# Kernel optimization log

Measured on AMD Instinct MI355X. Metric: run time of the kernel, lower is better.

Reference implementation:

```python
import jax, jax.numpy as jnp
import numpy as np

B, N, D, H = 2, 2048, 128, 16  # batch, seq, per-head dim, heads
ALL = D * H


def setup_inputs() -> dict:
    key = jax.random.key(0)
    ks = jax.random.split(key, 12)
    s = 0.02
    x = jax.random.normal(ks[0], (B, N, D), dtype=jnp.float32)
    mask = jax.random.randint(ks[1], (B, N), 0, 2, dtype=jnp.int32)
    Wq = jax.random.normal(ks[2], (D, ALL), dtype=jnp.float32) * s
    bq = jnp.zeros((ALL,), dtype=jnp.float32)
    Wk = jax.random.normal(ks[3], (D, ALL), dtype=jnp.float32) * s
    bk = jnp.zeros((ALL,), dtype=jnp.float32)
    Wv = jax.random.normal(ks[4], (D, ALL), dtype=jnp.float32) * s
    bv = jnp.zeros((ALL,), dtype=jnp.float32)
    Wo = jax.random.normal(ks[5], (ALL, D), dtype=jnp.float32) * s
    bo = jnp.zeros((D,), dtype=jnp.float32)
    return {"x": x, "mask": mask, "Wq": Wq, "bq": bq, "Wk": Wk, "bk": bk,
            "Wv": Wv, "bv": bv, "Wo": Wo, "bo": bo}


def reference(x, mask, Wq, bq, Wk, bk, Wv, bv, Wo, bo):
    b, n, d = x.shape
    h = ALL // d
    # project and split heads: [b, n, h, d] -> [b, h, n, d]
    q = (x @ Wq + bq).reshape(b, n, h, d).transpose(0, 2, 1, 3)
    k = (x @ Wk + bk).reshape(b, n, h, d).transpose(0, 2, 1, 3)
    v = (x @ Wv + bv).reshape(b, n, h, d).transpose(0, 2, 1, 3)
    scores = jnp.einsum('bhqd,bhkd->bhqk', q, k) / jnp.sqrt(jnp.float32(d))
    # key mask: [b,1,1,n]
    scores = jnp.where(mask[:, None, None, :] == 0, -jnp.inf, scores)
    attn = jax.nn.softmax(scores, axis=-1)  # dropout p=0.0 -> identity
    out = jnp.einsum('bhqk,bhkd->bhqd', attn, v)
    # query mask: [b,1,n,1]
    out = jnp.where(mask[:, None, :, None] == 0, 0.0, out)
    out = out.transpose(0, 2, 1, 3).reshape(b, n, h * d)
    return out @ Wo + bo
```

## Files before the change

### kernel.cpp

```cpp
#include <hip/hip_runtime.h>
#include <hip/hip_bf16.h>

#define B_   2
#define N_   2048
#define D_   128
#define H_   16
#define ALL_ 2048
#define M_   (B_*N_)
#define BH_  (B_*H_)

typedef __bf16 bf16;
typedef __bf16 bf16x8 __attribute__((ext_vector_type(8)));
typedef __bf16 bf16x4 __attribute__((ext_vector_type(4)));
typedef float  floatx4 __attribute__((ext_vector_type(4)));

#define MFMA32K(a,b,c) __builtin_amdgcn_mfma_f32_16x16x32_bf16((a),(b),(c),0,0,0)

__device__ inline void load_lds16(const bf16* g, bf16* l) {
    __builtin_amdgcn_global_load_lds((const __attribute__((address_space(1))) void*)g,
                                     (__attribute__((address_space(3))) void*)l, 16, 0, 0);
}

#define WAITCNT_VM(n) ((0xF << 8) | (0x7 << 4) | (n))


__global__ __launch_bounds__(256) void prep_weights(const float* __restrict__ x,
                                                    const float* __restrict__ Wq,
                                                    const float* __restrict__ Wk,
                                                    const float* __restrict__ Wv,
                                                    const float* __restrict__ Wo,
                                                    const int* __restrict__ mask,
                                                    bf16* __restrict__ Wqf,
                                                    bf16* __restrict__ Wkf,
                                                    bf16* __restrict__ Wvf,
                                                    bf16* __restrict__ Wof,
                                                    bf16* __restrict__ xf,
                                                    float* __restrict__ mbias) {
    __shared__ bf16 pw[16896];
    int bid = blockIdx.x, t = threadIdx.x;
    int lane = t & 63, wave = t >> 6;
    int lrow = lane & 15, quad = lane >> 4;

    if (bid < 192) {
        int m = bid / 64, rest = bid % 64;
        int cg = rest >> 1, kh = rest & 1;
        const float* W = (m == 0) ? Wq : (m == 1) ? Wk : Wv;
        bf16* Wf       = (m == 0) ? Wqf : (m == 1) ? Wkf : Wvf;
        int slot = t & 15, rowb = t >> 4;
#pragma unroll
        for (int i = 0; i < 4; i++) {
            int rl_ = rowb + i * 16;
            float4 v = *(const float4*)(W + (size_t)(kh * 64 + rl_) * 2048 + cg * 64 + slot * 4);
            bf16x4 o; o[0]=(bf16)v.x; o[1]=(bf16)v.y; o[2]=(bf16)v.z; o[3]=(bf16)v.w;
            *(bf16x4*)(&pw[rl_ * 68 + slot * 4]) = o;
        }
        __syncthreads();
        int ctl = wave;
#pragma unroll
        for (int kfl = 0; kfl < 2; kfl++) {
            bf16x8 w;
#pragma unroll
            for (int j = 0; j < 8; j++) w[j] = pw[(kfl * 32 + quad * 8 + j) * 68 + ctl * 16 + lrow];
            *(bf16x8*)(Wf + (size_t)((cg * 4 + ctl) * 4 + kh * 2 + kfl) * 512 + lane * 8) = w;
        }
    } else if (bid < 224) {
        int idx = bid - 192;
        int kb16 = idx >> 1, ch = idx & 1;
        int k0 = kb16 * 128;
        int slot = t & 15, rowb = t >> 4;
#pragma unroll
        for (int i = 0; i < 8; i++) {
            int r = rowb + i * 16;
            float4 v = *(const float4*)(Wo + (size_t)(k0 + r) * 128 + ch * 64 + slot * 4);
            bf16x4 o; o[0]=(bf16)v.x; o[1]=(bf16)v.y; o[2]=(bf16)v.z; o[3]=(bf16)v.w;
            *(bf16x4*)(&pw[r * 68 + slot * 4]) = o;
        }
        __syncthreads();
        int ctl = wave;
        int ct = ch * 4 + ctl;
#pragma unroll
        for (int kfl = 0; kfl < 4; kfl++) {
            bf16x8 w;
#pragma unroll
            for (int j = 0; j < 8; j++)
                w[j] = pw[(kfl * 32 + ((j >> 2) << 4) + quad * 4 + (j & 3)) * 68 + ctl * 16 + lrow];
            *(bf16x8*)(Wof + (size_t)(ct * 64 + kb16 * 4 + kfl) * 512 + lane * 8) = w;
        }
    } else if (bid < 352) {
        int idx = bid - 224, r0 = idx * 32;
        int slot = t & 31, rowb = t >> 5;
#pragma unroll
        for (int i = 0; i < 4; i++) {
            int r = rowb + i * 8;
            float4 v = *(const float4*)(x + (size_t)(r0 + r) * 128 + slot * 4);
            bf16x4 o; o[0]=(bf16)v.x; o[1]=(bf16)v.y; o[2]=(bf16)v.z; o[3]=(bf16)v.w;
            *(bf16x4*)(&pw[r * 136 + slot * 4]) = o;
        }
        __syncthreads();
        int rtl = wave >> 1;
        int kf2 = (wave & 1) * 2;
#pragma unroll
        for (int kfl = 0; kfl < 2; kfl++) {
            int kf = kf2 + kfl;
            bf16x8 w = *(const bf16x8*)(&pw[(rtl * 16 + lrow) * 136 + kf * 32 + quad * 8]);
            *(bf16x8*)(xf + (size_t)((idx * 2 + rtl) * 4 + kf) * 512 + lane * 8) = w;
        }
    } else {
        int e = (bid - 352) * 256 + t;
        mbias[e] = mask[e] ? 0.0f : -43.2808512f;
    }
}

__global__ __launch_bounds__(256) void qkv_proj(const bf16* __restrict__ xf,
                                                const float* __restrict__ bq,
                                                const float* __restrict__ bk,
                                                const float* __restrict__ bv,
                                                const bf16* __restrict__ Wqf,
                                                const bf16* __restrict__ Wkf,
                                                const bf16* __restrict__ Wvf,
                                                bf16* __restrict__ Qf,
                                                bf16* __restrict__ Kf,
                                                bf16* __restrict__ Vf) {
    __shared__ bf16 tile[64][72];

    int tid = threadIdx.x;
    int wave = tid >> 6, lane = tid & 63;
    int lrow = lane & 15, quad = lane >> 4;
    int r0b = blockIdx.x * 64;
    int c0 = blockIdx.y * 64;
    int cg4 = c0 >> 4;

    int rt = (r0b >> 4) + wave;
    bf16x8 a[4];
#pragma unroll
    for (int kf = 0; kf < 4; kf++)
        a[kf] = *(const bf16x8*)(xf + (size_t)(rt * 4 + kf) * 512 + lane * 8);

    int bb = r0b >> 11;
    int h  = c0 >> 7;
    int bhw = bb * 16 + h;
    int tile16 = (r0b & 2047) >> 4;
    int kbt = (r0b & 2047) >> 6;
    floatx4 zero4 = {0.f, 0.f, 0.f, 0.f};

#pragma unroll
    for (int z = 0; z < 3; z++) {
        const float* bias = (z == 0) ? bq : (z == 1) ? bk : bv;
        const bf16*  Wf   = (z == 0) ? Wqf : (z == 1) ? Wkf : Wvf;

        floatx4 acc[4] = {zero4, zero4, zero4, zero4};
#pragma unroll
        for (int kf = 0; kf < 4; kf++) {
#pragma unroll
            for (int nf = 0; nf < 4; nf++) {
                bf16x8 b = *(const bf16x8*)(Wf + (size_t)((cg4 + nf) * 4 + kf) * 512 + lane * 8);
                acc[nf] = MFMA32K(a[kf], b, acc[nf]);
            }
        }

#pragma unroll
        for (int nf = 0; nf < 4; nf++) {
            int col = nf * 16 + lrow;
            float bvv = bias[c0 + col];
#pragma unroll
            for (int r = 0; r < 4; r++) {
                int row = wave * 16 + quad * 4 + r;
                bf16 val = (bf16)(acc[nf][r] + bvv);
                if (z < 2) tile[row][col] = val;
                else       tile[col][row] = val;
            }
        }
        __syncthreads();

        if (z < 2) {
            bf16* dst = (z == 0) ? Qf : Kf;
            int s = wave;
            int kfbase = (c0 & 127) >> 5;
            size_t fbase = ((size_t)bhw * 128 + tile16 + s) * 4 + kfbase;
#pragma unroll
            for (int kfl = 0; kfl < 2; kfl++) {
                bf16x8 w = *(const bf16x8*)(&tile[s * 16 + lrow][kfl * 32 + quad * 8]);
                *(bf16x8*)(dst + (fbase + kfl) * 512 + lane * 8) = w;
            }
        } else {
            int nfl = wave;
            int nfbase = (c0 & 127) >> 4;
            size_t fbase = (((size_t)bhw * 32 + kbt) * 8 + (nfbase + nfl)) * 2;
#pragma unroll
            for (int g = 0; g < 2; g++) {
                bf16x4 a0 = *(const bf16x4*)(&tile[nfl * 16 + lrow][g * 32 + quad * 4]);
                bf16x4 a1 = *(const bf16x4*)(&tile[nfl * 16 + lrow][g * 32 + 16 + quad * 4]);
                bf16x8 w;
                w[0]=a0[0]; w[1]=a0[1]; w[2]=a0[2]; w[3]=a0[3];
                w[4]=a1[0]; w[5]=a1[1]; w[6]=a1[2]; w[7]=a1[3];
                *(bf16x8*)(Vf + (fbase + g) * 512 + lane * 8) = w;
            }
        }
        if (z < 2) __syncthreads();
    }
}

__global__ __launch_bounds__(256, 2) void flash_attn(const bf16* __restrict__ Qf,
                                                     const bf16* __restrict__ Kf,
                                                     const bf16* __restrict__ Vf,
                                                     const float* __restrict__ mbias,
                                                     const int* __restrict__ mask,
                                                     bf16* __restrict__ ctxf) {
    __shared__ bf16 sm[20480];
    float* mbL = (float*)&sm[16384];

    int tid = threadIdx.x;
    int wave = tid >> 6, lane = tid & 63;
    int lrow = lane & 15, quad = lane >> 4;
    int bid = blockIdx.x;
    int xcd = bid & 7, seq = bid >> 3;
    int bh  = xcd * 4 + (seq >> 4);
    int qblk = seq & 15;
    int b  = bh >> 4;
    int q0 = qblk * 128 + wave * 32;

    const float* mbp = mbias + b * N_;
    const bf16* kbase = Kf + (size_t)bh * 262144;
    const bf16* vbase = Vf + (size_t)bh * 262144;

    bf16x8 qf[2][4];
#pragma unroll
    for (int u = 0; u < 2; u++)
#pragma unroll
        for (int kf = 0; kf < 4; kf++)
            qf[u][kf] = *(const bf16x8*)(Qf + (size_t)(((size_t)bh * 128 + (q0 >> 4) + u) * 4 + kf) * 512 + lane * 8);

    bf16x8 ones;
#pragma unroll
    for (int j = 0; j < 8; j++) ones[j] = (bf16)1.0f;

    floatx4 zero4 = {0.f, 0.f, 0.f, 0.f};
    floatx4 O[2][8];
#pragma unroll
    for (int u = 0; u < 2; u++)
#pragma unroll
        for (int nf = 0; nf < 8; nf++) O[u][nf] = zero4;
    floatx4 Oext[2] = {zero4, zero4};

    const float scale = 0.12751742f;

#pragma unroll
    for (int i = 0; i < 4; i++) {
        int seg = wave * 4 + i;
        load_lds16(kbase + seg * 512 + lane * 8, &sm[seg * 512]);
    }
#pragma unroll
    for (int i = 0; i < 2; i++) {
        int seg = wave * 2 + i;
        load_lds16((const bf16*)(mbp + seg * 256) + lane * 8, (bf16*)(mbL + seg * 256));
    }

    for (int kb = 0; kb < 32; kb++) {
        int cur = (kb & 1) << 13;

        __builtin_amdgcn_s_waitcnt(WAITCNT_VM(0));
        __builtin_amdgcn_s_barrier();

        if (kb < 31) {
            int nxt = cur ^ 8192;
            const bf16* ksrc = kbase + (size_t)(kb + 1) * 8192;
#pragma unroll
            for (int i = 0; i < 4; i++) {
                int seg = wave * 4 + i;
                load_lds16(ksrc + seg * 512 + lane * 8, &sm[nxt + seg * 512]);
            }
        }

        const bf16* vsrc = vbase + (size_t)kb * 8192 + lane * 8;
        bf16x8 vreg[16];
#pragma unroll
        for (int f = 0; f < 16; f++)
            vreg[f] = *(const bf16x8*)(vsrc + f * 512);

        bf16x8 pf[2][2];
#pragma unroll
        for (int s = 0; s < 4; s++) {
            floatx4 S0 = zero4, S1 = zero4;
            __builtin_amdgcn_s_setprio(1);
#pragma unroll
            for (int kf = 0; kf < 4; kf++) {
                bf16x8 kfr = *(const bf16x8*)(&sm[cur + ((s * 4 + kf) * 64 + lane) * 8]);
                S0 = MFMA32K(kfr, qf[0][kf], S0);
                S1 = MFMA32K(kfr, qf[1][kf], S1);
            }
            __builtin_amdgcn_s_setprio(0);
            float4 mb4 = *(const float4*)(mbL + kb * 64 + s * 16 + quad * 4);
            const float* mbr = (const float*)&mb4;
            int g = s >> 1, o = (s & 1) * 4;
#pragma unroll
            for (int r = 0; r < 4; r++) {
                float p0 = __builtin_amdgcn_exp2f(fmaf(S0[r], scale, mbr[r]));
                float p1 = __builtin_amdgcn_exp2f(fmaf(S1[r], scale, mbr[r]));
                pf[0][g][o + r] = (bf16)p0;
                pf[1][g][o + r] = (bf16)p1;
            }
        }

#pragma unroll
        for (int g = 0; g < 2; g++) {
            Oext[0] = MFMA32K(ones, pf[0][g], Oext[0]);
            Oext[1] = MFMA32K(ones, pf[1][g], Oext[1]);
        }

        __builtin_amdgcn_s_setprio(1);
#pragma unroll
        for (int nf = 0; nf < 8; nf++) {
#pragma unroll
            for (int g = 0; g < 2; g++) {
                O[0][nf] = MFMA32K(vreg[nf * 2 + g], pf[0][g], O[0][nf]);
                O[1][nf] = MFMA32K(vreg[nf * 2 + g], pf[1][g], O[1][nf]);
            }
        }
        __builtin_amdgcn_s_setprio(0);
    }

    const int* mp = mask + b * N_;
    int h4 = (bh & 15) * 4;
    size_t qtb = (size_t)b * 128 + (q0 >> 4);
#pragma unroll
    for (int u = 0; u < 2; u++) {
        float lsum = Oext[u][0];
        int q = q0 + u * 16 + lrow;
        float rl = (mp[q] && lsum > 0.f) ? (1.0f / lsum) : 0.f;
#pragma unroll
        for (int g = 0; g < 4; g++) {
            bf16x8 w;
#pragma unroll
            for (int j = 0; j < 4; j++) {
                w[j]     = (bf16)(O[u][2 * g][j]     * rl);
                w[j + 4] = (bf16)(O[u][2 * g + 1][j] * rl);
            }
            *(bf16x8*)(ctxf + ((qtb + u) * 64 + h4 + g) * 512 + lane * 8) = w;
        }
    }
}

__global__ __launch_bounds__(128) void out_proj(const bf16* __restrict__ ctxf,
                                                const bf16* __restrict__ Wof,
                                                const float* __restrict__ bo,
                                                float* __restrict__ out) {
    __shared__ float red[512];
    int tid = threadIdx.x;
    int wave = tid >> 6, lane = tid & 63;
    int lrow = lane & 15, quad = lane >> 4;
    int qt = blockIdx.x;
    int ct = blockIdx.y * 2;
    int r0 = qt * 16, c0 = ct * 16;

    floatx4 zero4 = {0.f, 0.f, 0.f, 0.f};
    floatx4 acc[2] = {zero4, zero4};
    const bf16* ap = ctxf + ((size_t)qt * 64 + wave * 32) * 512 + lane * 8;
    const bf16* b0 = Wof + ((size_t)ct * 64 + wave * 32) * 512 + lane * 8;
    const bf16* b1 = b0 + (size_t)64 * 512;
#pragma unroll 4
    for (int kf = 0; kf < 32; kf++) {
        bf16x8 a  = *(const bf16x8*)(ap + (size_t)kf * 512);
        bf16x8 w0 = *(const bf16x8*)(b0 + (size_t)kf * 512);
        bf16x8 w1 = *(const bf16x8*)(b1 + (size_t)kf * 512);
        acc[0] = MFMA32K(a, w0, acc[0]);
        acc[1] = MFMA32K(a, w1, acc[1]);
    }
    if (wave == 1) {
#pragma unroll
        for (int nf = 0; nf < 2; nf++)
#pragma unroll
            for (int r = 0; r < 4; r++)
                red[nf * 256 + r * 64 + lane] = acc[nf][r];
    }
    __syncthreads();
    if (wave == 0) {
#pragma unroll
        for (int nf = 0; nf < 2; nf++) {
            int col = c0 + nf * 16 + lrow;
            float bv = bo[col];
#pragma unroll
            for (int r = 0; r < 4; r++) {
                int m = r0 + quad * 4 + r;
                out[(size_t)m * 128 + col] = acc[nf][r] + red[nf * 256 + r * 64 + lane] + bv;
            }
        }
    }
}

extern "C" void kernel_launch(void* const* d_in, const int* in_sizes, int n_in,
                              void* d_out, int out_size, void* d_ws, size_t ws_size,
                              hipStream_t stream) {
    const float* x    = (const float*)d_in[0];
    const int*   mask = (const int*)d_in[1];
    const float* Wq   = (const float*)d_in[2];
    const float* bq   = (const float*)d_in[3];
    const float* Wk   = (const float*)d_in[4];
    const float* bk   = (const float*)d_in[5];
    const float* Wv   = (const float*)d_in[6];
    const float* bv   = (const float*)d_in[7];
    const float* Wo   = (const float*)d_in[8];
    const float* bo   = (const float*)d_in[9];
    float* out = (float*)d_out;

    char* ws = (char*)d_ws;
    size_t off = 0;
    bf16* Wqf = (bf16*)(ws + off); off += (size_t)262144 * 2;
    bf16* Wkf = (bf16*)(ws + off); off += (size_t)262144 * 2;
    bf16* Wvf = (bf16*)(ws + off); off += (size_t)262144 * 2;
    bf16* Wof = (bf16*)(ws + off); off += (size_t)262144 * 2;
    bf16* xf  = (bf16*)(ws + off); off += (size_t)524288 * 2;
    size_t qkv_elems = (size_t)BH_ * N_ * 128;
    bf16* Qf  = (bf16*)(ws + off); off += qkv_elems * 2;
    bf16* Kf  = (bf16*)(ws + off); off += qkv_elems * 2;
    bf16* Vf  = (bf16*)(ws + off); off += qkv_elems * 2;
    bf16* ctxf = (bf16*)(ws + off); off += (size_t)M_ * ALL_ * 2;
    float* mbias = (float*)(ws + off); off += (size_t)B_ * N_ * 4;
    (void)ws_size; (void)in_sizes; (void)n_in; (void)out_size;

    prep_weights<<<368, 256, 0, stream>>>(x, Wq, Wk, Wv, Wo, mask,
                                          Wqf, Wkf, Wvf, Wof, xf, mbias);

    qkv_proj<<<dim3(64, 32), 256, 0, stream>>>(xf, bq, bk, bv, Wqf, Wkf, Wvf,
                                               Qf, Kf, Vf);

    flash_attn<<<512, 256, 0, stream>>>(Qf, Kf, Vf, mbias, mask, ctxf);

    out_proj<<<dim3(256, 4), 128, 0, stream>>>(ctxf, Wof, bo, out);
}
```

Baseline: 173.0 us.

## Triple-buffer K tiles in LDS and split the PV update into two halves

The flash-attention kernel moves from a double to a triple LDS buffer for K, prefetching two tiles ahead. It now waits only on older loads (vmcnt 4) instead of draining all outstanding loads each iteration, and V register loads are issued before the K prefetch. The QK/softmax/PV chain in each 64-key block is split into two 32-key halves, so PV MFMAs for the first half can interleave with the score computation of the second. LDS use per block grows, which may limit occupancy at two blocks per CU, and the waitcnt count ties correctness to the exact number of outstanding loads.

```diff
diff --git a/kernel.cpp b/kernel.cpp
--- a/kernel.cpp
+++ b/kernel.cpp
@@ -206,8 +206,8 @@
                                                      const float* __restrict__ mbias,
                                                      const int* __restrict__ mask,
                                                      bf16* __restrict__ ctxf) {
-    __shared__ bf16 sm[20480];
-    float* mbL = (float*)&sm[16384];
+    __shared__ bf16 sm[24576];
+    __shared__ float mbL[2048];
 
     int tid = threadIdx.x;
     int wave = tid >> 6, lane = tid & 63;
@@ -254,32 +254,37 @@
         int seg = wave * 2 + i;
         load_lds16((const bf16*)(mbp + seg * 256) + lane * 8, (bf16*)(mbL + seg * 256));
     }
-
+#pragma unroll
+    for (int i = 0; i < 4; i++) {
+        int seg = wave * 4 + i;
+        load_lds16(kbase + 8192 + seg * 512 + lane * 8, &sm[8192 + seg * 512]);
+    }
+    __builtin_amdgcn_s_waitcnt(WAITCNT_VM(0));
+
+    int cur = 0;
     for (int kb = 0; kb < 32; kb++) {
-        int cur = (kb & 1) << 13;
-
-        __builtin_amdgcn_s_waitcnt(WAITCNT_VM(0));
+        __builtin_amdgcn_s_waitcnt(WAITCNT_VM(4));
         __builtin_amdgcn_s_barrier();
 
-        if (kb < 31) {
-            int nxt = cur ^ 8192;
-            const bf16* ksrc = kbase + (size_t)(kb + 1) * 8192;
+        const bf16* vsrc = vbase + (size_t)kb * 8192 + lane * 8;
+        bf16x8 vreg[16];
+#pragma unroll
+        for (int f = 0; f < 16; f++)
+            vreg[f] = *(const bf16x8*)(vsrc + f * 512);
+
+        if (kb < 30) {
+            int dst = cur + 16384; if (dst >= 24576) dst -= 24576;
+            const bf16* ksrc = kbase + (size_t)(kb + 2) * 8192;
 #pragma unroll
             for (int i = 0; i < 4; i++) {
                 int seg = wave * 4 + i;
-                load_lds16(ksrc + seg * 512 + lane * 8, &sm[nxt + seg * 512]);
-            }
-        }
-
-        const bf16* vsrc = vbase + (size_t)kb * 8192 + lane * 8;
-        bf16x8 vreg[16];
-#pragma unroll
-        for (int f = 0; f < 16; f++)
-            vreg[f] = *(const bf16x8*)(vsrc + f * 512);
-
-        bf16x8 pf[2][2];
-#pragma unroll
-        for (int s = 0; s < 4; s++) {
+                load_lds16(ksrc + seg * 512 + lane * 8, &sm[dst + seg * 512]);
+            }
+        }
+
+        bf16x8 pfa[2];
+#pragma unroll
+        for (int s = 0; s < 2; s++) {
             floatx4 S0 = zero4, S1 = zero4;
             __builtin_amdgcn_s_setprio(1);
 #pragma unroll
@@ -291,32 +296,61 @@
             __builtin_amdgcn_s_setprio(0);
             float4 mb4 = *(const float4*)(mbL + kb * 64 + s * 16 + quad * 4);
             const float* mbr = (const float*)&mb4;
-            int g = s >> 1, o = (s & 1) * 4;
+            int o = s * 4;
 #pragma unroll
             for (int r = 0; r < 4; r++) {
                 float p0 = __builtin_amdgcn_exp2f(fmaf(S0[r], scale, mbr[r]));
                 float p1 = __builtin_amdgcn_exp2f(fmaf(S1[r], scale, mbr[r]));
-                pf[0][g][o + r] = (bf16)p0;
-                pf[1][g][o + r] = (bf16)p1;
-            }
-        }
-
-#pragma unroll
-        for (int g = 0; g < 2; g++) {
-            Oext[0] = MFMA32K(ones, pf[0][g], Oext[0]);
-            Oext[1] = MFMA32K(ones, pf[1][g], Oext[1]);
+                pfa[0][o + r] = (bf16)p0;
+                pfa[1][o + r] = (bf16)p1;
+            }
         }
 
         __builtin_amdgcn_s_setprio(1);
+        Oext[0] = MFMA32K(ones, pfa[0], Oext[0]);
+        Oext[1] = MFMA32K(ones, pfa[1], Oext[1]);
 #pragma unroll
         for (int nf = 0; nf < 8; nf++) {
-#pragma unroll
-            for (int g = 0; g < 2; g++) {
-                O[0][nf] = MFMA32K(vreg[nf * 2 + g], pf[0][g], O[0][nf]);
-                O[1][nf] = MFMA32K(vreg[nf * 2 + g], pf[1][g], O[1][nf]);
-            }
+            O[0][nf] = MFMA32K(vreg[nf * 2], pfa[0], O[0][nf]);
+            O[1][nf] = MFMA32K(vreg[nf * 2], pfa[1], O[1][nf]);
         }
         __builtin_amdgcn_s_setprio(0);
+
+        bf16x8 pfb[2];
+#pragma unroll
+        for (int s = 2; s < 4; s++) {
+            floatx4 S0 = zero4, S1 = zero4;
+            __builtin_amdgcn_s_setprio(1);
+#pragma unroll
+            for (int kf = 0; kf < 4; kf++) {
+                bf16x8 kfr = *(const bf16x8*)(&sm[cur + ((s * 4 + kf) * 64 + lane) * 8]);
+                S0 = MFMA32K(kfr, qf[0][kf], S0);
+                S1 = MFMA32K(kfr, qf[1][kf], S1);
+            }
+            __builtin_amdgcn_s_setprio(0);
+            float4 mb4 = *(const float4*)(mbL + kb * 64 + s * 16 + quad * 4);
+            const float* mbr = (const float*)&mb4;
+            int o = (s - 2) * 4;
+#pragma unroll
+            for (int r = 0; r < 4; r++) {
+                float p0 = __builtin_amdgcn_exp2f(fmaf(S0[r], scale, mbr[r]));
+                float p1 = __builtin_amdgcn_exp2f(fmaf(S1[r], scale, mbr[r]));
+                pfb[0][o + r] = (bf16)p0;
+                pfb[1][o + r] = (bf16)p1;
+            }
+        }
+
+        __builtin_amdgcn_s_setprio(1);
+        Oext[0] = MFMA32K(ones, pfb[0], Oext[0]);
+        Oext[1] = MFMA32K(ones, pfb[1], Oext[1]);
+#pragma unroll
+        for (int nf = 0; nf < 8; nf++) {
+            O[0][nf] = MFMA32K(vreg[nf * 2 + 1], pfb[0], O[0][nf]);
+            O[1][nf] = MFMA32K(vreg[nf * 2 + 1], pfb[1], O[1][nf]);
+        }
+        __builtin_amdgcn_s_setprio(0);
+
+        cur += 8192; if (cur == 24576) cur = 0;
     }
 
     const int* mp = mask + b * N_;
```

After: 174.3 us. Within noise of the previous version (+0.8%).

## Load K directly into registers and drop LDS staging and barriers in flash attention

Applied to the files above, without the earlier changes.

The attention kernel no longer stages K tiles and the mask bias in shared memory through async global-to-LDS copies with a per-iteration barrier. Each wave now reads its K fragments straight from global memory into registers, prefetching one sub-tile ahead, and reads the mask bias directly from global. The PV MFMA work is split into two halves so the first half issues midway through the score computation. This removes LDS traffic and block-wide synchronisation, at the cost of four waves each re-reading the same K data from global/L2 and higher register pressure.

```diff
diff --git a/kernel.cpp b/kernel.cpp
--- a/kernel.cpp
+++ b/kernel.cpp
@@ -20,8 +20,6 @@
     __builtin_amdgcn_global_load_lds((const __attribute__((address_space(1))) void*)g,
                                      (__attribute__((address_space(3))) void*)l, 16, 0, 0);
 }
-
-#define WAITCNT_VM(n) ((0xF << 8) | (0x7 << 4) | (n))
 
 
 __global__ __launch_bounds__(256) void prep_weights(const float* __restrict__ x,
@@ -206,9 +204,6 @@
                                                      const float* __restrict__ mbias,
                                                      const int* __restrict__ mask,
                                                      bf16* __restrict__ ctxf) {
-    __shared__ bf16 sm[20480];
-    float* mbL = (float*)&sm[16384];
-
     int tid = threadIdx.x;
     int wave = tid >> 6, lane = tid & 63;
     int lrow = lane & 15, quad = lane >> 4;
@@ -220,8 +215,8 @@
     int q0 = qblk * 128 + wave * 32;
 
     const float* mbp = mbias + b * N_;
-    const bf16* kbase = Kf + (size_t)bh * 262144;
-    const bf16* vbase = Vf + (size_t)bh * 262144;
+    const bf16* kbase = Kf + (size_t)bh * 262144 + lane * 8;
+    const bf16* vbase = Vf + (size_t)bh * 262144 + lane * 8;
 
     bf16x8 qf[2][4];
 #pragma unroll
@@ -244,77 +239,71 @@
 
     const float scale = 0.12751742f;
 
-#pragma unroll
-    for (int i = 0; i < 4; i++) {
-        int seg = wave * 4 + i;
-        load_lds16(kbase + seg * 512 + lane * 8, &sm[seg * 512]);
-    }
-#pragma unroll
-    for (int i = 0; i < 2; i++) {
-        int seg = wave * 2 + i;
-        load_lds16((const bf16*)(mbp + seg * 256) + lane * 8, (bf16*)(mbL + seg * 256));
-    }
-
-    for (int kb = 0; kb < 32; kb++) {
-        int cur = (kb & 1) << 13;
-
-        __builtin_amdgcn_s_waitcnt(WAITCNT_VM(0));
-        __builtin_amdgcn_s_barrier();
-
-        if (kb < 31) {
-            int nxt = cur ^ 8192;
-            const bf16* ksrc = kbase + (size_t)(kb + 1) * 8192;
-#pragma unroll
-            for (int i = 0; i < 4; i++) {
-                int seg = wave * 4 + i;
-                load_lds16(ksrc + seg * 512 + lane * 8, &sm[nxt + seg * 512]);
-            }
-        }
-
-        const bf16* vsrc = vbase + (size_t)kb * 8192 + lane * 8;
+    bf16x8 kcur[4];
+#pragma unroll
+    for (int kf = 0; kf < 4; kf++)
+        kcur[kf] = *(const bf16x8*)(kbase + kf * 512);
+
+    for (int t = 0; t < 32; t++) {
+        const bf16* vsrc = vbase + (size_t)t * 8192;
         bf16x8 vreg[16];
 #pragma unroll
         for (int f = 0; f < 16; f++)
             vreg[f] = *(const bf16x8*)(vsrc + f * 512);
 
-        bf16x8 pf[2][2];
+        bf16x8 pfa[2], pfb[2];
 #pragma unroll
         for (int s = 0; s < 4; s++) {
+            int tn = (s == 3) ? ((t < 31) ? t + 1 : 31) : t;
+            int sn = (s + 1) & 3;
+            const bf16* knsrc = kbase + (size_t)tn * 8192 + sn * 2048;
+            bf16x8 knxt[4];
+#pragma unroll
+            for (int kf = 0; kf < 4; kf++)
+                knxt[kf] = *(const bf16x8*)(knsrc + kf * 512);
+
             floatx4 S0 = zero4, S1 = zero4;
             __builtin_amdgcn_s_setprio(1);
 #pragma unroll
             for (int kf = 0; kf < 4; kf++) {
-                bf16x8 kfr = *(const bf16x8*)(&sm[cur + ((s * 4 + kf) * 64 + lane) * 8]);
-                S0 = MFMA32K(kfr, qf[0][kf], S0);
-                S1 = MFMA32K(kfr, qf[1][kf], S1);
+                S0 = MFMA32K(kcur[kf], qf[0][kf], S0);
+                S1 = MFMA32K(kcur[kf], qf[1][kf], S1);
             }
             __builtin_amdgcn_s_setprio(0);
-            float4 mb4 = *(const float4*)(mbL + kb * 64 + s * 16 + quad * 4);
+
+            float4 mb4 = *(const float4*)(mbp + t * 64 + s * 16 + quad * 4);
             const float* mbr = (const float*)&mb4;
-            int g = s >> 1, o = (s & 1) * 4;
+            int o = (s & 1) * 4;
 #pragma unroll
             for (int r = 0; r < 4; r++) {
                 float p0 = __builtin_amdgcn_exp2f(fmaf(S0[r], scale, mbr[r]));
                 float p1 = __builtin_amdgcn_exp2f(fmaf(S1[r], scale, mbr[r]));
-                pf[0][g][o + r] = (bf16)p0;
-                pf[1][g][o + r] = (bf16)p1;
-            }
-        }
-
-#pragma unroll
-        for (int g = 0; g < 2; g++) {
-            Oext[0] = MFMA32K(ones, pf[0][g], Oext[0]);
-            Oext[1] = MFMA32K(ones, pf[1][g], Oext[1]);
+                if (s < 2) { pfa[0][o + r] = (bf16)p0; pfa[1][o + r] = (bf16)p1; }
+                else       { pfb[0][o + r] = (bf16)p0; pfb[1][o + r] = (bf16)p1; }
+            }
+#pragma unroll
+            for (int kf = 0; kf < 4; kf++) kcur[kf] = knxt[kf];
+
+            if (s == 1) {
+                __builtin_amdgcn_s_setprio(1);
+                Oext[0] = MFMA32K(ones, pfa[0], Oext[0]);
+                Oext[1] = MFMA32K(ones, pfa[1], Oext[1]);
+#pragma unroll
+                for (int nf = 0; nf < 8; nf++) {
+                    O[0][nf] = MFMA32K(vreg[nf * 2], pfa[0], O[0][nf]);
+                    O[1][nf] = MFMA32K(vreg[nf * 2], pfa[1], O[1][nf]);
+                }
+                __builtin_amdgcn_s_setprio(0);
+            }
         }
 
         __builtin_amdgcn_s_setprio(1);
+        Oext[0] = MFMA32K(ones, pfb[0], Oext[0]);
+        Oext[1] = MFMA32K(ones, pfb[1], Oext[1]);
 #pragma unroll
         for (int nf = 0; nf < 8; nf++) {
-#pragma unroll
-            for (int g = 0; g < 2; g++) {
-                O[0][nf] = MFMA32K(vreg[nf * 2 + g], pf[0][g], O[0][nf]);
-                O[1][nf] = MFMA32K(vreg[nf * 2 + g], pf[1][g], O[1][nf]);
-            }
+            O[0][nf] = MFMA32K(vreg[nf * 2 + 1], pfb[0], O[0][nf]);
+            O[1][nf] = MFMA32K(vreg[nf * 2 + 1], pfb[1], O[1][nf]);
         }
         __builtin_amdgcn_s_setprio(0);
     }
```

New measurement: 189.8 us. 1.1x slower.

## Use 8 waves of 16 query rows in flash attention and split V loads

Applied to the files above, without the earlier changes.

The flash attention block now runs 512 threads, with each wave owning 16 query rows instead of 32. This halves the per-wave O accumulators and Q fragments. The V fragment loads are split into two halves, each interleaved with half of the score computation, which shrinks live V registers and lets loads overlap MFMA work. This raises occupancy and latency hiding, but each V fragment loaded from global memory now feeds half as many MFMAs, so V traffic per block doubles.

```diff
diff --git a/kernel.cpp b/kernel.cpp
--- a/kernel.cpp
+++ b/kernel.cpp
@@ -200,14 +200,14 @@
     }
 }
 
-__global__ __launch_bounds__(256, 2) void flash_attn(const bf16* __restrict__ Qf,
+__global__ __launch_bounds__(512, 4) void flash_attn(const bf16* __restrict__ Qf,
                                                      const bf16* __restrict__ Kf,
                                                      const bf16* __restrict__ Vf,
                                                      const float* __restrict__ mbias,
                                                      const int* __restrict__ mask,
                                                      bf16* __restrict__ ctxf) {
-    __shared__ bf16 sm[20480];
-    float* mbL = (float*)&sm[16384];
+    __shared__ bf16 sm[16384];
+    __shared__ float mbL[2048];
 
     int tid = threadIdx.x;
     int wave = tid >> 6, lane = tid & 63;
@@ -217,126 +217,131 @@
     int bh  = xcd * 4 + (seq >> 4);
     int qblk = seq & 15;
     int b  = bh >> 4;
-    int q0 = qblk * 128 + wave * 32;
+    int q0 = qblk * 128 + wave * 16;
 
     const float* mbp = mbias + b * N_;
     const bf16* kbase = Kf + (size_t)bh * 262144;
-    const bf16* vbase = Vf + (size_t)bh * 262144;
-
-    bf16x8 qf[2][4];
-#pragma unroll
-    for (int u = 0; u < 2; u++)
-#pragma unroll
-        for (int kf = 0; kf < 4; kf++)
-            qf[u][kf] = *(const bf16x8*)(Qf + (size_t)(((size_t)bh * 128 + (q0 >> 4) + u) * 4 + kf) * 512 + lane * 8);
+    const bf16* vbase = Vf + (size_t)bh * 262144 + lane * 8;
+
+    bf16x8 qf[4];
+#pragma unroll
+    for (int kf = 0; kf < 4; kf++)
+        qf[kf] = *(const bf16x8*)(Qf + (size_t)(((size_t)bh * 128 + (q0 >> 4)) * 4 + kf) * 512 + lane * 8);
 
     bf16x8 ones;
 #pragma unroll
     for (int j = 0; j < 8; j++) ones[j] = (bf16)1.0f;
 
     floatx4 zero4 = {0.f, 0.f, 0.f, 0.f};
-    floatx4 O[2][8];
-#pragma unroll
-    for (int u = 0; u < 2; u++)
-#pragma unroll
-        for (int nf = 0; nf < 8; nf++) O[u][nf] = zero4;
-    floatx4 Oext[2] = {zero4, zero4};
+    floatx4 O[8];
+#pragma unroll
+    for (int nf = 0; nf < 8; nf++) O[nf] = zero4;
+    floatx4 Oext = zero4;
 
     const float scale = 0.12751742f;
 
-#pragma unroll
-    for (int i = 0; i < 4; i++) {
-        int seg = wave * 4 + i;
-        load_lds16(kbase + seg * 512 + lane * 8, &sm[seg * 512]);
-    }
 #pragma unroll
     for (int i = 0; i < 2; i++) {
         int seg = wave * 2 + i;
-        load_lds16((const bf16*)(mbp + seg * 256) + lane * 8, (bf16*)(mbL + seg * 256));
-    }
-
-    for (int kb = 0; kb < 32; kb++) {
-        int cur = (kb & 1) << 13;
+        load_lds16(kbase + seg * 512 + lane * 8, &sm[seg * 512]);
+    }
+    load_lds16((const bf16*)(mbp + wave * 256) + lane * 8, (bf16*)(mbL + wave * 256));
+
+    for (int t = 0; t < 32; t++) {
+        int cur = (t & 1) << 13;
 
         __builtin_amdgcn_s_waitcnt(WAITCNT_VM(0));
         __builtin_amdgcn_s_barrier();
 
-        if (kb < 31) {
+        if (t < 31) {
             int nxt = cur ^ 8192;
-            const bf16* ksrc = kbase + (size_t)(kb + 1) * 8192;
-#pragma unroll
-            for (int i = 0; i < 4; i++) {
-                int seg = wave * 4 + i;
+            const bf16* ksrc = kbase + (size_t)(t + 1) * 8192;
+#pragma unroll
+            for (int i = 0; i < 2; i++) {
+                int seg = wave * 2 + i;
                 load_lds16(ksrc + seg * 512 + lane * 8, &sm[nxt + seg * 512]);
             }
         }
 
-        const bf16* vsrc = vbase + (size_t)kb * 8192 + lane * 8;
-        bf16x8 vreg[16];
-#pragma unroll
-        for (int f = 0; f < 16; f++)
-            vreg[f] = *(const bf16x8*)(vsrc + f * 512);
-
-        bf16x8 pf[2][2];
-#pragma unroll
-        for (int s = 0; s < 4; s++) {
-            floatx4 S0 = zero4, S1 = zero4;
+        const bf16* vsrc = vbase + (size_t)t * 8192;
+        bf16x8 v0[8];
+#pragma unroll
+        for (int nf = 0; nf < 8; nf++)
+            v0[nf] = *(const bf16x8*)(vsrc + (nf * 2) * 512);
+
+        bf16x8 pfa;
+#pragma unroll
+        for (int s = 0; s < 2; s++) {
+            floatx4 S = zero4;
             __builtin_amdgcn_s_setprio(1);
 #pragma unroll
             for (int kf = 0; kf < 4; kf++) {
                 bf16x8 kfr = *(const bf16x8*)(&sm[cur + ((s * 4 + kf) * 64 + lane) * 8]);
-                S0 = MFMA32K(kfr, qf[0][kf], S0);
-                S1 = MFMA32K(kfr, qf[1][kf], S1);
+                S = MFMA32K(kfr, qf[kf], S);
             }
             __builtin_amdgcn_s_setprio(0);
-            float4 mb4 = *(const float4*)(mbL + kb * 64 + s * 16 + quad * 4);
+            float4 mb4 = *(const float4*)(mbL + t * 64 + s * 16 + quad * 4);
             const float* mbr = (const float*)&mb4;
-            int g = s >> 1, o = (s & 1) * 4;
-#pragma unroll
-            for (int r = 0; r < 4; r++) {
-                float p0 = __builtin_amdgcn_exp2f(fmaf(S0[r], scale, mbr[r]));
-                float p1 = __builtin_amdgcn_exp2f(fmaf(S1[r], scale, mbr[r]));
-                pf[0][g][o + r] = (bf16)p0;
-                pf[1][g][o + r] = (bf16)p1;
-            }
-        }
-
-#pragma unroll
-        for (int g = 0; g < 2; g++) {
-            Oext[0] = MFMA32K(ones, pf[0][g], Oext[0]);
-            Oext[1] = MFMA32K(ones, pf[1][g], Oext[1]);
+            int o = s * 4;
+#pragma unroll
+            for (int r = 0; r < 4; r++)
+                pfa[o + r] = (bf16)__builtin_amdgcn_exp2f(fmaf(S[r], scale, mbr[r]));
         }
 
         __builtin_amdgcn_s_setprio(1);
-#pragma unroll
-        for (int nf = 0; nf < 8; nf++) {
-#pragma unroll
-            for (int g = 0; g < 2; g++) {
-                O[0][nf] = MFMA32K(vreg[nf * 2 + g], pf[0][g], O[0][nf]);
-                O[1][nf] = MFMA32K(vreg[nf * 2 + g], pf[1][g], O[1][nf]);
-            }
-        }
+        Oext = MFMA32K(ones, pfa, Oext);
+#pragma unroll
+        for (int nf = 0; nf < 8; nf++)
+            O[nf] = MFMA32K(v0[nf], pfa, O[nf]);
+        __builtin_amdgcn_s_setprio(0);
+
+        bf16x8 v1[8];
+#pragma unroll
+        for (int nf = 0; nf < 8; nf++)
+            v1[nf] = *(const bf16x8*)(vsrc + (nf * 2 + 1) * 512);
+
+        bf16x8 pfb;
+#pragma unroll
+        for (int s = 2; s < 4; s++) {
+            floatx4 S = zero4;
+            __builtin_amdgcn_s_setprio(1);
+#pragma unroll
+            for (int kf = 0; kf < 4; kf++) {
+                bf16x8 kfr = *(const bf16x8*)(&sm[cur + ((s * 4 + kf) * 64 + lane) * 8]);
+                S = MFMA32K(kfr, qf[kf], S);
+            }
+            __builtin_amdgcn_s_setprio(0);
+            float4 mb4 = *(const float4*)(mbL + t * 64 + s * 16 + quad * 4);
+            const float* mbr = (const float*)&mb4;
+            int o = (s - 2) * 4;
+#pragma unroll
+            for (int r = 0; r < 4; r++)
+                pfb[o + r] = (bf16)__builtin_amdgcn_exp2f(fmaf(S[r], scale, mbr[r]));
+        }
+
+        __builtin_amdgcn_s_setprio(1);
+        Oext = MFMA32K(ones, pfb, Oext);
+#pragma unroll
+        for (int nf = 0; nf < 8; nf++)
+            O[nf] = MFMA32K(v1[nf], pfb, O[nf]);
         __builtin_amdgcn_s_setprio(0);
     }
 
     const int* mp = mask + b * N_;
     int h4 = (bh & 15) * 4;
     size_t qtb = (size_t)b * 128 + (q0 >> 4);
-#pragma unroll
-    for (int u = 0; u < 2; u++) {
-        float lsum = Oext[u][0];
-        int q = q0 + u * 16 + lrow;
-        float rl = (mp[q] && lsum > 0.f) ? (1.0f / lsum) : 0.f;
-#pragma unroll
-        for (int g = 0; g < 4; g++) {
-            bf16x8 w;
-#pragma unroll
-            for (int j = 0; j < 4; j++) {
-                w[j]     = (bf16)(O[u][2 * g][j]     * rl);
-                w[j + 4] = (bf16)(O[u][2 * g + 1][j] * rl);
-            }
-            *(bf16x8*)(ctxf + ((qtb + u) * 64 + h4 + g) * 512 + lane * 8) = w;
-        }
+    float lsum = Oext[0];
+    int q = q0 + lrow;
+    float rl = (mp[q] && lsum > 0.f) ? (1.0f / lsum) : 0.f;
+#pragma unroll
+    for (int g = 0; g < 4; g++) {
+        bf16x8 w;
+#pragma unroll
+        for (int j = 0; j < 4; j++) {
+            w[j]     = (bf16)(O[2 * g][j]     * rl);
+            w[j + 4] = (bf16)(O[2 * g + 1][j] * rl);
+        }
+        *(bf16x8*)(ctxf + (qtb * 64 + h4 + g) * 512 + lane * 8) = w;
     }
 }
 
@@ -423,7 +428,7 @@
     qkv_proj<<<dim3(64, 32), 256, 0, stream>>>(xf, bq, bk, bv, Wqf, Wkf, Wvf,
                                                Qf, Kf, Vf);
 
-    flash_attn<<<512, 256, 0, stream>>>(Qf, Kf, Vf, mbias, mask, ctxf);
+    flash_attn<<<512, 512, 0, stream>>>(Qf, Kf, Vf, mbias, mask, ctxf);
 
     out_proj<<<dim3(256, 4), 128, 0, stream>>>(ctxf, Wof, bo, out);
 }
```

Result: slower. 186.6 us (+7.9%).
